# Optimization experiments

Hardware: AMD Instinct MI355X
Metric: run time of the kernel (lower is better)

Reference implementation:

```python
import jax, jax.numpy as jnp
import numpy as np

N = 50000          # nodes
E = 800000         # edges (avg degree 16)
NODE_IN, NODE_OUT = 64, 96
EDGE_IN, EDGE_OUT = 32, 32
CONV = [192, 192]  # hidden_conv_sizes
LIN = [192]        # hidden_linear_sizes
NUM_CLASSES = 2


def _linear_init(k, fan_in, fan_out):
    s = 1.0 / np.sqrt(fan_in)
    kw, kb = jax.random.split(k)
    W = jax.random.uniform(kw, (fan_in, fan_out), jnp.float32, -s, s)
    b = jax.random.uniform(kb, (fan_out,), jnp.float32, -s, s)
    return W, b


def setup_inputs() -> dict:
    key = jax.random.key(0)
    ks = jax.random.split(key, 10)
    node_feats = jax.random.normal(ks[0], (N, NODE_IN), jnp.float32)
    edge_feats = jax.random.normal(ks[1], (E, EDGE_IN), jnp.float32)
    src = jax.random.randint(ks[2], (E,), 0, N)
    dst = jax.random.randint(ks[3], (E,), 0, N)
    Wn, bn = _linear_init(ks[4], NODE_IN, NODE_OUT)
    We, be = _linear_init(ks[5], EDGE_IN, EDGE_OUT)
    Wc0, bc0 = _linear_init(ks[6], NODE_OUT + EDGE_OUT, CONV[0])
    Wc1, bc1 = _linear_init(ks[7], CONV[0], CONV[1])
    Wl0, bl0 = _linear_init(ks[8], CONV[1], LIN[0])
    Wo, bo = _linear_init(ks[9], LIN[0], NUM_CLASSES)
    return dict(node_feats=node_feats, edge_feats=edge_feats,
                Wn=Wn, bn=bn, We=We, be=be,
                Wc0=Wc0, bc0=bc0, Wc1=Wc1, bc1=bc1,
                Wl0=Wl0, bl0=bl0, Wo=Wo, bo=bo,
                src=src, dst=dst)


def reference(node_feats, edge_feats, Wn, bn, We, be, Wc0, bc0, Wc1, bc1,
              Wl0, bl0, Wo, bo, src, dst):
    ones = jnp.ones((E,), jnp.float32)
    deg_in = jnp.clip(jax.ops.segment_sum(ones, dst, num_segments=N), 1.0)
    deg_out = jnp.clip(jax.ops.segment_sum(ones, src, num_segments=N), 1.0)
    inv_in = jax.lax.rsqrt(deg_in)    # D_in^{-1/2}
    inv_out = jax.lax.rsqrt(deg_out)  # D_out^{-1/2}

    # EdgeLayer: per-edge linear, mean-aggregated onto destination nodes
    eh = edge_feats @ We + be                                   # [E, EDGE_OUT]
    edge_h = jax.nn.relu(
        jax.ops.segment_sum(eh, dst, num_segments=N) / deg_in[:, None])

    # NodeEmbeddingLayer: per-node linear
    node_h = jax.nn.relu(node_feats @ Wn + bn)                  # [N, NODE_OUT]

    h = jnp.concatenate([edge_h, node_h], axis=1)               # [N, EDGE_OUT+NODE_OUT]

    # dgl GraphConv (norm='both'): D_in^{-1/2} A D_out^{-1/2} h W + b
    # dropout is identity in eval mode
    for W, b in ((Wc0, bc0), (Wc1, bc1)):
        msg = (h * inv_out[:, None])[src]                       # [E, d] gather
        agg = jax.ops.segment_sum(msg, dst, num_segments=N) * inv_in[:, None]
        h = jax.nn.relu(agg @ W + b)

    h = jax.nn.relu(h @ Wl0 + bl0)
    return h @ Wo + bo                                          # [N, NUM_CLASSES]
```

## Files before the change

kernel.cpp:

```cpp
#include <hip/hip_runtime.h>

#define NN 50000
#define NE 800000
#define CAP 64

#define NPB 128
#define NBKT 391
#define NBKT_PAD 512
#define BCAP 3072
#define CHUNK 4096
#define GW4E 12500

typedef unsigned short u16;
typedef unsigned int u32;
typedef unsigned long long u64;
typedef __attribute__((ext_vector_type(8))) short bf8_t;
typedef __attribute__((ext_vector_type(4))) float f4_t;

__device__ __forceinline__ u16 f2b(float f) {
    unsigned u = __float_as_uint(f);
    unsigned r = u + 0x7FFF + ((u >> 16) & 1);
    return (u16)(r >> 16);
}

__device__ __forceinline__ void pack_one(const float* __restrict__ W, u16* __restrict__ Wp,
                                         int idx, int KS) {
    int l = idx & 63;
    int s = (idx >> 6) % KS;
    int t = (idx >> 6) / KS;
    int col = t * 16 + (l & 15);
    int krow = s * 32 + ((l >> 4) * 8);
    u16 tmp[8] __attribute__((aligned(16)));
#pragma unroll
    for (int j = 0; j < 8; ++j) tmp[j] = f2b(W[(size_t)(krow + j) * 192 + col]);
    *(uint4*)(Wp + (size_t)idx * 8) = *(const uint4*)tmp;
}

__global__ __launch_bounds__(256) void partition_pack_k(
    const int* __restrict__ src, const int* __restrict__ dst,
    int* __restrict__ deg_out, int* __restrict__ bktc,
    u64* __restrict__ part, int E,
    const float* __restrict__ Wc0, const float* __restrict__ Wc1,
    const float* __restrict__ Wl0,
    u16* __restrict__ Wp0, u16* __restrict__ Wp1, u16* __restrict__ Wp2) {
    const int PBLK = (E + CHUNK - 1) / CHUNK;
    if (blockIdx.x >= PBLK) {
        int idx = (blockIdx.x - PBLK) * 256 + threadIdx.x;
        if (idx < 3072) pack_one(Wc0, Wp0, idx, 4);
        else if (idx < 7680) pack_one(Wc1, Wp1, idx - 3072, 6);
        else if (idx < 12288) pack_one(Wl0, Wp2, idx - 7680, 6);
        return;
    }

    __shared__ unsigned cnt[NBKT_PAD];
    __shared__ unsigned base[NBKT_PAD];
    __shared__ unsigned cur[NBKT_PAD];
    __shared__ unsigned gbase[NBKT_PAD];
    __shared__ unsigned wtot[4];
    __shared__ u64 staged[CHUNK];

    const int tid = threadIdx.x;
    const int lane = tid & 63;
    const int wid = tid >> 6;
    const int e0 = blockIdx.x * CHUNK;
    const int n = min(CHUNK, E - e0);

    for (int i = tid; i < NBKT_PAD; i += 256) cnt[i] = 0;
    __syncthreads();

    for (int i = tid; i < n; i += 256) {
        int d = dst[e0 + i];
        atomicAdd(&cnt[d >> 7], 1u);
    }
    __syncthreads();

    {
        unsigned a = cnt[2 * tid];
        unsigned b = cnt[2 * tid + 1];
        unsigned ps = a + b;
        unsigned inc = ps;
#pragma unroll
        for (int d = 1; d < 64; d <<= 1) {
            unsigned v = __shfl_up(inc, d);
            if (lane >= d) inc += v;
        }
        if (lane == 63) wtot[wid] = inc;
        __syncthreads();
        unsigned wb = 0;
#pragma unroll
        for (int k = 0; k < 4; ++k) wb += (k < wid) ? wtot[k] : 0;
        unsigned eb = wb + inc - ps;
        base[2 * tid] = eb;
        base[2 * tid + 1] = eb + a;
        cur[2 * tid] = eb;
        cur[2 * tid + 1] = eb + a;
    }
    __syncthreads();

    for (int i = tid; i < n; i += 256) {
        int e = e0 + i;
        int d = dst[e];
        int s = src[e];
        atomicAdd(deg_out + s, 1);
        unsigned p = atomicAdd(&cur[d >> 7], 1u);
        staged[p] = ((u64)(unsigned)e << 32) | (((u32)d << 16) | (u32)s);
    }
    __syncthreads();

    for (int b = tid; b < NBKT; b += 256) {
        unsigned c = cur[b] - base[b];
        if (c) gbase[b] = (unsigned)atomicAdd(&bktc[b], (int)c);
    }
    __syncthreads();

    for (int i = tid; i < n; i += 256) {
        u64 v = staged[i];
        int b = (int)((v >> 16) & 0xffffu) >> 7;
        unsigned idx = gbase[b] + ((unsigned)i - base[b]);
        if (idx < BCAP) part[(size_t)b * BCAP + idx] = v;
    }
}

__global__ __launch_bounds__(256) void fill_k(
    const u64* __restrict__ part, const int* __restrict__ bktc,
    const int* __restrict__ deg_out,
    int* __restrict__ csr_src, int* __restrict__ csr_eid,
    int* __restrict__ din,
    float* __restrict__ inv_in, float* __restrict__ inv_out,
    float* __restrict__ inv_mean, float* __restrict__ bcoef, int n) {
    __shared__ unsigned cur[NPB];
    const int tid = threadIdx.x;
    const int b = blockIdx.x;
    const int node0 = b << 7;
    if (tid < NPB) cur[tid] = 0;
    __syncthreads();

    const int cnt = min(bktc[b], BCAP);
    const u64* p = part + (size_t)b * BCAP;
    for (int i = tid; i < cnt; i += 256) {
        u64 v = p[i];
        int s = (int)(v & 0xffffu);
        int d = (int)((v >> 16) & 0xffffu);
        int e = (int)(v >> 32);
        unsigned q = atomicAdd(&cur[d & (NPB - 1)], 1u);
        if (q < CAP) {
            csr_src[((size_t)d << 6) + q] = s;
            csr_eid[((size_t)d << 6) + q] = e;
        }
    }
    __syncthreads();
    if (tid < NPB) {
        int node = node0 + tid;
        if (node < n) {
            unsigned cq = min(cur[tid], (unsigned)CAP);
            din[node] = (int)cq;
            int end = (cq <= 32u) ? 32 : 64;
            for (int q = (int)cq; q < end; ++q)
                csr_eid[((size_t)node << 6) + q] = 0;
            float di = fmaxf((float)cq, 1.0f);
            float dq = fmaxf((float)deg_out[node], 1.0f);
            inv_in[node]   = 1.0f / sqrtf(di);
            inv_out[node]  = 1.0f / sqrtf(dq);
            inv_mean[node] = 1.0f / di;
            bcoef[node]    = (cq > 0u) ? 1.0f : 0.0f;
        }
    }
}

__global__ __launch_bounds__(256) void edge_node_k(
    const float* __restrict__ ef, const int* __restrict__ csr_eid,
    const int* __restrict__ deg,
    const float* __restrict__ inv_mean, const float* __restrict__ bcoef,
    const float* __restrict__ inv_out,
    const float* __restrict__ We, const float* __restrict__ be,
    const float* __restrict__ nf, const float* __restrict__ Wn,
    const float* __restrict__ bn,
    u16* __restrict__ h0, int n) {
    __shared__ float sv[4][32];
    __shared__ float s_in[32 * 64];
    const int tid = threadIdx.x;
    const int lane = tid & 63;
    const int w = tid >> 6;

    if (blockIdx.x < GW4E) {
        const int node = __builtin_amdgcn_readfirstlane(blockIdx.x * 4 + w);
        const int beg = node << 6;
        const int cnt = deg[node];
        const int g = lane >> 4;
        const int c = lane & 15;

        float ax = 0.0f, ay = 0.0f;
        {
            int eidv[8];
#pragma unroll
            for (int j = 0; j < 8; ++j) eidv[j] = csr_eid[beg + 4 * j + g];
            float2 v[8];
#pragma unroll
            for (int j = 0; j < 8; ++j)
                v[j] = *(const float2*)(ef + (size_t)eidv[j] * 32 + 2 * c);
#pragma unroll
            for (int j = 0; j < 8; ++j)
                if (4 * j + g < cnt) { ax += v[j].x; ay += v[j].y; }
        }
        if (cnt > 32) {
            int eidv[8];
#pragma unroll
            for (int j = 0; j < 8; ++j) eidv[j] = csr_eid[beg + 32 + 4 * j + g];
            float2 v[8];
#pragma unroll
            for (int j = 0; j < 8; ++j)
                v[j] = *(const float2*)(ef + (size_t)eidv[j] * 32 + 2 * c);
#pragma unroll
            for (int j = 0; j < 8; ++j)
                if (32 + 4 * j + g < cnt) { ax += v[j].x; ay += v[j].y; }
        }
        ax += __shfl_down(ax, 16); ay += __shfl_down(ay, 16);
        ax += __shfl_down(ax, 32); ay += __shfl_down(ay, 32);
        if (lane < 16) {
            float im = inv_mean[node];
            float2 o; o.x = ax * im; o.y = ay * im;
            *(float2*)&sv[w][2 * c] = o;
        }
        int col = lane & 31;
        float s = 0.0f;
#pragma unroll 8
        for (int k = 0; k < 32; ++k)
            s = fmaf(sv[w][k], We[k * 32 + col], s);
        if (lane < 32) {
            float v = fmaxf(s + be[col] * bcoef[node], 0.0f) * inv_out[node];
            h0[(size_t)node * 128 + col] = f2b(v);
        }
        return;
    }

    const int row0 = (blockIdx.x - GW4E) * 32;
    for (int i = tid; i < 512; i += 256) {
        int m = i >> 4;
        int kv = i & 15;
        int row = min(row0 + m, n - 1);
        float4 v = *(const float4*)(nf + (size_t)row * 64 + kv * 4);
        *(float4*)(s_in + m * 64 + kv * 4) = v;
    }
    __syncthreads();

    int f0 = lane, f1 = lane + 64;
    bool fok1 = (f1 < 96);
    int ff1 = fok1 ? f1 : 0;
    float bv0 = bn[f0], bv1 = bn[ff1];

    const float* s_my = s_in + w * 8 * 64;
    float acc0[8], acc1[8];
#pragma unroll
    for (int m = 0; m < 8; ++m) { acc0[m] = 0.0f; acc1[m] = 0.0f; }

    for (int k = 0; k < 64; k += 4) {
        float wv[4][2];
#pragma unroll
        for (int j = 0; j < 4; ++j) {
            wv[j][0] = Wn[(k + j) * 96 + f0];
            wv[j][1] = Wn[(k + j) * 96 + ff1];
        }
#pragma unroll
        for (int m = 0; m < 8; ++m) {
            float4 a = *(const float4*)(s_my + m * 64 + k);
            acc0[m] = fmaf(a.x, wv[0][0], acc0[m]);
            acc0[m] = fmaf(a.y, wv[1][0], acc0[m]);
            acc0[m] = fmaf(a.z, wv[2][0], acc0[m]);
            acc0[m] = fmaf(a.w, wv[3][0], acc0[m]);
            acc1[m] = fmaf(a.x, wv[0][1], acc1[m]);
            acc1[m] = fmaf(a.y, wv[1][1], acc1[m]);
            acc1[m] = fmaf(a.z, wv[2][1], acc1[m]);
            acc1[m] = fmaf(a.w, wv[3][1], acc1[m]);
        }
    }

#pragma unroll
    for (int m = 0; m < 8; ++m) {
        int row = row0 + w * 8 + m;
        if (row < n) {
            float pm = inv_out[row];
            float v0 = fmaxf(acc0[m] + bv0, 0.0f) * pm;
            h0[(size_t)row * 128 + 32 + f0] = f2b(v0);
            if (fok1) {
                float v1 = fmaxf(acc1[m] + bv1, 0.0f) * pm;
                h0[(size_t)row * 128 + 32 + f1] = f2b(v1);
            }
        }
    }
}

template <int D, int LPT>
__global__ __launch_bounds__(256) void gather_b2_k(
    const u16* __restrict__ h, const int* __restrict__ csr,
    const int* __restrict__ deg, const float* __restrict__ inv_in,
    u16* __restrict__ agg) {
    constexpr int ACT = D / LPT;
    constexpr int NW = LPT / 2;
    const int lane = threadIdx.x & 63;
    const int node = __builtin_amdgcn_readfirstlane(blockIdx.x * 4 + (threadIdx.x >> 6));
    const int beg = node << 6;
    const int cnt = deg[node];
    const int off = (lane < ACT ? lane : ACT - 1) * LPT;

    float acc[LPT];
#pragma unroll
    for (int j = 0; j < LPT; ++j) acc[j] = 0.0f;

    const int nb = cnt >> 4;
    int idx[16];
    if (nb > 0) {
#pragma unroll
        for (int j = 0; j < 16; ++j) idx[j] = csr[beg + j];
    }
    for (int b = 0; b < nb; ++b) {
        unsigned lv[16][NW];
#pragma unroll
        for (int j = 0; j < 16; ++j) {
            const unsigned* p = (const unsigned*)(h + (size_t)idx[j] * D + off);
            if constexpr (NW == 2) {
                uint2 t = *(const uint2*)p;
                lv[j][0] = t.x; lv[j][1] = t.y;
            } else {
                lv[j][0] = *p;
            }
        }
        int nidx[16];
        const int nbase = beg + (b + 1) * 16;
        if (b + 1 < nb) {
#pragma unroll
            for (int j = 0; j < 16; ++j) nidx[j] = csr[nbase + j];
        }
#pragma unroll
        for (int j = 0; j < 16; ++j)
#pragma unroll
            for (int q = 0; q < NW; ++q) {
                unsigned u = lv[j][q];
                acc[2 * q]     += __uint_as_float(u << 16);
                acc[2 * q + 1] += __uint_as_float(u & 0xffff0000u);
            }
        if (b + 1 < nb) {
#pragma unroll
            for (int j = 0; j < 16; ++j) idx[j] = nidx[j];
        }
    }

    int tb = beg + (nb << 4);
    int rem = cnt & 15;
    if (rem >= 8) {
        int ti[8];
#pragma unroll
        for (int j = 0; j < 8; ++j) ti[j] = csr[tb + j];
        unsigned lv[8][NW];
#pragma unroll
        for (int j = 0; j < 8; ++j) {
            const unsigned* p = (const unsigned*)(h + (size_t)ti[j] * D + off);
            if constexpr (NW == 2) {
                uint2 t = *(const uint2*)p;
                lv[j][0] = t.x; lv[j][1] = t.y;
            } else {
                lv[j][0] = *p;
            }
        }
#pragma unroll
        for (int j = 0; j < 8; ++j)
#pragma unroll
            for (int q = 0; q < NW; ++q) {
                unsigned u = lv[j][q];
                acc[2 * q]     += __uint_as_float(u << 16);
                acc[2 * q + 1] += __uint_as_float(u & 0xffff0000u);
            }
        tb += 8;
        rem -= 8;
    }
    for (int t = 0; t < rem; ++t) {
        const unsigned* p = (const unsigned*)(h + (size_t)csr[tb + t] * D + off);
#pragma unroll
        for (int q = 0; q < NW; ++q) {
            unsigned u = p[q];
            acc[2 * q]     += __uint_as_float(u << 16);
            acc[2 * q + 1] += __uint_as_float(u & 0xffff0000u);
        }
    }

    if (lane < ACT) {
        float sc = inv_in[node];
        unsigned o[NW];
#pragma unroll
        for (int q = 0; q < NW; ++q)
            o[q] = (unsigned)f2b(acc[2 * q] * sc) | ((unsigned)f2b(acc[2 * q + 1] * sc) << 16);
        unsigned* dp = (unsigned*)(agg + (size_t)node * D + off);
        if constexpr (NW == 2) {
            uint2 t; t.x = o[0]; t.y = o[1];
            *(uint2*)dp = t;
        } else {
            *dp = o[0];
        }
    }
}

template <int K>
__global__ __launch_bounds__(256) void mfma_gemm_k(
    const u16* __restrict__ A, const u16* __restrict__ Wp,
    const float* __restrict__ bias, const float* __restrict__ posts,
    u16* __restrict__ outB, int n) {
    constexpr int KS = K / 32;
    const int tid = threadIdx.x;
    const int lane = tid & 63;
    const int w = tid >> 6;
    const int row0 = blockIdx.x * 16;
    const int arow = row0 + (lane & 15);
    const int kbase = (lane >> 4) * 8;

    f4_t acc[3];
#pragma unroll
    for (int o = 0; o < 3; ++o) acc[o] = (f4_t){0.f, 0.f, 0.f, 0.f};

    const u16* ap = A + (size_t)arow * K + kbase;
#pragma unroll
    for (int s = 0; s < KS; ++s) {
        bf8_t af = *(const bf8_t*)(ap + s * 32);
#pragma unroll
        for (int o = 0; o < 3; ++o) {
            int t = w * 3 + o;
            bf8_t bf = *(const bf8_t*)(Wp + (size_t)((t * KS + s) * 64 + lane) * 8);
            acc[o] = __builtin_amdgcn_mfma_f32_16x16x32_bf16(af, bf, acc[o], 0, 0, 0);
        }
    }

    const int drow = row0 + (lane >> 4) * 4;
    const int dcol = lane & 15;
    float pm[4];
#pragma unroll
    for (int r = 0; r < 4; ++r) pm[r] = posts[drow + r];
#pragma unroll
    for (int o = 0; o < 3; ++o) {
        int col = (w * 3 + o) * 16 + dcol;
        float bv = bias[col];
#pragma unroll
        for (int r = 0; r < 4; ++r) {
            float v = fmaxf(acc[o][r] + bv, 0.0f) * pm[r];
            outB[(size_t)(drow + r) * 192 + col] = f2b(v);
        }
    }
}

__global__ __launch_bounds__(256) void mfma_fused_k(
    const u16* __restrict__ A,
    const u16* __restrict__ Wp1, const float* __restrict__ b1,
    const u16* __restrict__ Wp2, const float* __restrict__ b2,
    const float* __restrict__ Wo, const float* __restrict__ bo,
    float* __restrict__ out, int n) {
    constexpr int KS = 6;
    constexpr int S = 200;
    __shared__ float sbuf[16 * S];
    __shared__ float s_head[16][17][2];

    const int tid = threadIdx.x;
    const int lane = tid & 63;
    const int w = tid >> 6;
    const int row0 = blockIdx.x * 16;
    const int arow = row0 + (lane & 15);
    const int kbase = (lane >> 4) * 8;
    const int drow = (lane >> 4) * 4;
    const int dcol = lane & 15;

    f4_t acc[3];
#pragma unroll
    for (int o = 0; o < 3; ++o) acc[o] = (f4_t){0.f, 0.f, 0.f, 0.f};

    const u16* ap = A + (size_t)arow * 192 + kbase;
#pragma unroll
    for (int s = 0; s < KS; ++s) {
        bf8_t af = *(const bf8_t*)(ap + s * 32);
#pragma unroll
        for (int o = 0; o < 3; ++o) {
            int t = w * 3 + o;
            bf8_t bf = *(const bf8_t*)(Wp1 + (size_t)((t * KS + s) * 64 + lane) * 8);
            acc[o] = __builtin_amdgcn_mfma_f32_16x16x32_bf16(af, bf, acc[o], 0, 0, 0);
        }
    }

    u16* h2 = (u16*)sbuf;
#pragma unroll
    for (int o = 0; o < 3; ++o) {
        int col = (w * 3 + o) * 16 + dcol;
        float bv = b1[col];
#pragma unroll
        for (int r = 0; r < 4; ++r)
            h2[(drow + r) * S + col] = f2b(fmaxf(acc[o][r] + bv, 0.0f));
    }
    __syncthreads();

#pragma unroll
    for (int o = 0; o < 3; ++o) acc[o] = (f4_t){0.f, 0.f, 0.f, 0.f};
    const u16* hp = h2 + (lane & 15) * S + kbase;
#pragma unroll
    for (int s = 0; s < KS; ++s) {
        bf8_t af = *(const bf8_t*)(hp + s * 32);
#pragma unroll
        for (int o = 0; o < 3; ++o) {
            int t = w * 3 + o;
            bf8_t bf = *(const bf8_t*)(Wp2 + (size_t)((t * KS + s) * 64 + lane) * 8);
            acc[o] = __builtin_amdgcn_mfma_f32_16x16x32_bf16(af, bf, acc[o], 0, 0, 0);
        }
    }
    __syncthreads();

#pragma unroll
    for (int o = 0; o < 3; ++o) {
        int col = (w * 3 + o) * 16 + dcol;
        float bv = b2[col];
#pragma unroll
        for (int r = 0; r < 4; ++r)
            sbuf[(drow + r) * S + col] = fmaxf(acc[o][r] + bv, 0.0f);
    }
    __syncthreads();

    {
        int r = tid >> 4;
        int seg = tid & 15;
        const float* hr = sbuf + r * S + seg * 12;
        const float* wor = Wo + seg * 24;
        float p0 = 0.0f, p1 = 0.0f;
#pragma unroll
        for (int c = 0; c < 12; ++c) {
            float hv = hr[c];
            p0 = fmaf(hv, wor[c * 2 + 0], p0);
            p1 = fmaf(hv, wor[c * 2 + 1], p1);
        }
        s_head[r][seg][0] = p0;
        s_head[r][seg][1] = p1;
    }
    __syncthreads();
    if (tid < 32) {
        int r = tid >> 1, c = tid & 1;
        float sum = bo[c];
#pragma unroll
        for (int g = 0; g < 16; ++g) sum += s_head[r][g][c];
        int row = row0 + r;
        if (row < n) out[(size_t)row * 2 + c] = sum;
    }
}

extern "C" void kernel_launch(void* const* d_in, const int* in_sizes, int n_in,
                              void* d_out, int out_size, void* d_ws, size_t ws_size,
                              hipStream_t stream) {
    const float* node_feats = (const float*)d_in[0];
    const float* edge_feats = (const float*)d_in[1];
    const float* Wn  = (const float*)d_in[2];
    const float* bn  = (const float*)d_in[3];
    const float* We  = (const float*)d_in[4];
    const float* be  = (const float*)d_in[5];
    const float* Wc0 = (const float*)d_in[6];
    const float* bc0 = (const float*)d_in[7];
    const float* Wc1 = (const float*)d_in[8];
    const float* bc1 = (const float*)d_in[9];
    const float* Wl0 = (const float*)d_in[10];
    const float* bl0 = (const float*)d_in[11];
    const float* Wo  = (const float*)d_in[12];
    const float* bo  = (const float*)d_in[13];
    const int* src = (const int*)d_in[14];
    const int* dst = (const int*)d_in[15];
    float* out = (float*)d_out;

    const int N = NN, E = NE;

    int* dout      = (int*)d_ws;
    int* bktc      = dout + N;
    int* din       = bktc + NBKT_PAD;
    int* csr_src   = din + N;
    int* csr_eid   = csr_src + (size_t)CAP * N;
    float* inv_in   = (float*)(csr_eid + (size_t)CAP * N);
    float* inv_out  = inv_in + N;
    float* inv_mean = inv_out + N;
    float* bcoef    = inv_mean + N;
    u16* h0   = (u16*)(bcoef + N);
    u16* aggA = h0 + (size_t)128 * N;
    u16* h1   = aggA + (size_t)128 * N;
    u16* aggB = h1 + (size_t)192 * N;
    u16* Wp0  = aggB + (size_t)192 * N;
    u16* Wp1  = Wp0 + 128 * 192;
    u16* Wp2  = Wp1 + 192 * 192;
    u64* part = (u64*)h1;

    hipMemsetAsync(d_ws, 0, (size_t)(N + NBKT_PAD) * sizeof(int), stream);

    const int PBLK = (E + CHUNK - 1) / CHUNK;
    const int GB16 = N / 16;
    const int GB32 = (N + 31) / 32;

    partition_pack_k<<<dim3(PBLK + 48), dim3(256), 0, stream>>>(
        src, dst, dout, bktc, part, E, Wc0, Wc1, Wl0, Wp0, Wp1, Wp2);
    fill_k<<<dim3(NBKT), dim3(256), 0, stream>>>(part, bktc, dout, csr_src, csr_eid,
                                                 din, inv_in, inv_out, inv_mean, bcoef, N);

    edge_node_k<<<dim3(GW4E + GB32), dim3(256), 0, stream>>>(
        edge_feats, csr_eid, din, inv_mean, bcoef, inv_out, We, be,
        node_feats, Wn, bn, h0, N);

    gather_b2_k<128, 2><<<dim3(GW4E), dim3(256), 0, stream>>>(h0, csr_src, din, inv_in, aggA);
    mfma_gemm_k<128><<<dim3(GB16), dim3(256), 0, stream>>>(aggA, Wp0, bc0, inv_out, h1, N);

    gather_b2_k<192, 4><<<dim3(GW4E), dim3(256), 0, stream>>>(h1, csr_src, din, inv_in, aggB);
    mfma_fused_k<<<dim3(GB16), dim3(256), 0, stream>>>(aggB, Wp1, bc1, Wp2, bl0, Wo, bo,
                                                       out, N);
}
```

Before: 407.2 us.

## Fuse neighbor gather with MFMA GEMM per 16-node tile via shared memory

Merges each graph-conv gather kernel with its following MFMA GEMM into one 1024-thread block. Each of the 16 waves aggregates one node into an LDS tile, then 12 waves each compute one 16-column output slab. This removes the aggA/aggB intermediate round trips through global memory and two kernel launches. In exchange, the cross-iteration index prefetch is dropped, 4 waves sit idle during the GEMM phase, and the large blocks with barriers may lower occupancy and latency hiding for the irregular gathers.

New measurement: 424.6 us. 1.04x slower.

```diff
diff --git a/kernel.cpp b/kernel.cpp
--- a/kernel.cpp
+++ b/kernel.cpp
@@ -289,169 +289,100 @@
     }
 }
 
-template <int D, int LPT>
-__global__ __launch_bounds__(256) void gather_b2_k(
-    const u16* __restrict__ h, const int* __restrict__ csr,
+__global__ __launch_bounds__(1024) void conv0_k(
+    const u16* __restrict__ h0, const int* __restrict__ csr,
     const int* __restrict__ deg, const float* __restrict__ inv_in,
-    u16* __restrict__ agg) {
-    constexpr int ACT = D / LPT;
-    constexpr int NW = LPT / 2;
-    const int lane = threadIdx.x & 63;
-    const int node = __builtin_amdgcn_readfirstlane(blockIdx.x * 4 + (threadIdx.x >> 6));
-    const int beg = node << 6;
-    const int cnt = deg[node];
-    const int off = (lane < ACT ? lane : ACT - 1) * LPT;
-
-    float acc[LPT];
-#pragma unroll
-    for (int j = 0; j < LPT; ++j) acc[j] = 0.0f;
-
-    const int nb = cnt >> 4;
-    int idx[16];
-    if (nb > 0) {
-#pragma unroll
-        for (int j = 0; j < 16; ++j) idx[j] = csr[beg + j];
-    }
-    for (int b = 0; b < nb; ++b) {
-        unsigned lv[16][NW];
-#pragma unroll
-        for (int j = 0; j < 16; ++j) {
-            const unsigned* p = (const unsigned*)(h + (size_t)idx[j] * D + off);
-            if constexpr (NW == 2) {
-                uint2 t = *(const uint2*)p;
-                lv[j][0] = t.x; lv[j][1] = t.y;
-            } else {
-                lv[j][0] = *p;
-            }
-        }
-        int nidx[16];
-        const int nbase = beg + (b + 1) * 16;
-        if (b + 1 < nb) {
-#pragma unroll
-            for (int j = 0; j < 16; ++j) nidx[j] = csr[nbase + j];
-        }
-#pragma unroll
-        for (int j = 0; j < 16; ++j)
-#pragma unroll
-            for (int q = 0; q < NW; ++q) {
-                unsigned u = lv[j][q];
-                acc[2 * q]     += __uint_as_float(u << 16);
-                acc[2 * q + 1] += __uint_as_float(u & 0xffff0000u);
-            }
-        if (b + 1 < nb) {
-#pragma unroll
-            for (int j = 0; j < 16; ++j) idx[j] = nidx[j];
-        }
-    }
-
-    int tb = beg + (nb << 4);
-    int rem = cnt & 15;
-    if (rem >= 8) {
-        int ti[8];
-#pragma unroll
-        for (int j = 0; j < 8; ++j) ti[j] = csr[tb + j];
-        unsigned lv[8][NW];
-#pragma unroll
-        for (int j = 0; j < 8; ++j) {
-            const unsigned* p = (const unsigned*)(h + (size_t)ti[j] * D + off);
-            if constexpr (NW == 2) {
-                uint2 t = *(const uint2*)p;
-                lv[j][0] = t.x; lv[j][1] = t.y;
-            } else {
-                lv[j][0] = *p;
-            }
-        }
-#pragma unroll
-        for (int j = 0; j < 8; ++j)
-#pragma unroll
-            for (int q = 0; q < NW; ++q) {
-                unsigned u = lv[j][q];
-                acc[2 * q]     += __uint_as_float(u << 16);
-                acc[2 * q + 1] += __uint_as_float(u & 0xffff0000u);
-            }
-        tb += 8;
-        rem -= 8;
-    }
-    for (int t = 0; t < rem; ++t) {
-        const unsigned* p = (const unsigned*)(h + (size_t)csr[tb + t] * D + off);
-#pragma unroll
-        for (int q = 0; q < NW; ++q) {
-            unsigned u = p[q];
-            acc[2 * q]     += __uint_as_float(u << 16);
-            acc[2 * q + 1] += __uint_as_float(u & 0xffff0000u);
-        }
-    }
-
-    if (lane < ACT) {
-        float sc = inv_in[node];
-        unsigned o[NW];
-#pragma unroll
-        for (int q = 0; q < NW; ++q)
-            o[q] = (unsigned)f2b(acc[2 * q] * sc) | ((unsigned)f2b(acc[2 * q + 1] * sc) << 16);
-        unsigned* dp = (unsigned*)(agg + (size_t)node * D + off);
-        if constexpr (NW == 2) {
-            uint2 t; t.x = o[0]; t.y = o[1];
-            *(uint2*)dp = t;
-        } else {
-            *dp = o[0];
-        }
-    }
-}
-
-template <int K>
-__global__ __launch_bounds__(256) void mfma_gemm_k(
-    const u16* __restrict__ A, const u16* __restrict__ Wp,
-    const float* __restrict__ bias, const float* __restrict__ posts,
-    u16* __restrict__ outB, int n) {
-    constexpr int KS = K / 32;
+    const u16* __restrict__ Wp, const float* __restrict__ bias,
+    const float* __restrict__ posts, u16* __restrict__ h1) {
+    constexpr int KS = 4, ST = 136;
+    __shared__ u16 tile[16 * ST];
     const int tid = threadIdx.x;
     const int lane = tid & 63;
     const int w = tid >> 6;
     const int row0 = blockIdx.x * 16;
-    const int arow = row0 + (lane & 15);
-    const int kbase = (lane >> 4) * 8;
-
-    f4_t acc[3];
-#pragma unroll
-    for (int o = 0; o < 3; ++o) acc[o] = (f4_t){0.f, 0.f, 0.f, 0.f};
-
-    const u16* ap = A + (size_t)arow * K + kbase;
-#pragma unroll
-    for (int s = 0; s < KS; ++s) {
-        bf8_t af = *(const bf8_t*)(ap + s * 32);
-#pragma unroll
-        for (int o = 0; o < 3; ++o) {
-            int t = w * 3 + o;
-            bf8_t bf = *(const bf8_t*)(Wp + (size_t)((t * KS + s) * 64 + lane) * 8);
-            acc[o] = __builtin_amdgcn_mfma_f32_16x16x32_bf16(af, bf, acc[o], 0, 0, 0);
-        }
-    }
-
-    const int drow = row0 + (lane >> 4) * 4;
-    const int dcol = lane & 15;
-    float pm[4];
-#pragma unroll
-    for (int r = 0; r < 4; ++r) pm[r] = posts[drow + r];
-#pragma unroll
-    for (int o = 0; o < 3; ++o) {
-        int col = (w * 3 + o) * 16 + dcol;
+    const int node = __builtin_amdgcn_readfirstlane(row0 + w);
+    const int beg = node << 6;
+    const int cnt = deg[node];
+    const int off = lane * 2;
+
+    float a0 = 0.0f, a1 = 0.0f;
+    {
+        const int nb = cnt >> 4;
+        for (int b = 0; b < nb; ++b) {
+            int idx[16];
+#pragma unroll
+            for (int j = 0; j < 16; ++j) idx[j] = csr[beg + b * 16 + j];
+            unsigned lv[16];
+#pragma unroll
+            for (int j = 0; j < 16; ++j)
+                lv[j] = *(const unsigned*)(h0 + (size_t)idx[j] * 128 + off);
+#pragma unroll
+            for (int j = 0; j < 16; ++j) {
+                a0 += __uint_as_float(lv[j] << 16);
+                a1 += __uint_as_float(lv[j] & 0xffff0000u);
+            }
+        }
+        int tb = beg + (nb << 4);
+        int rem = cnt & 15;
+        if (rem >= 8) {
+            int ti[8];
+#pragma unroll
+            for (int j = 0; j < 8; ++j) ti[j] = csr[tb + j];
+            unsigned lv[8];
+#pragma unroll
+            for (int j = 0; j < 8; ++j)
+                lv[j] = *(const unsigned*)(h0 + (size_t)ti[j] * 128 + off);
+#pragma unroll
+            for (int j = 0; j < 8; ++j) {
+                a0 += __uint_as_float(lv[j] << 16);
+                a1 += __uint_as_float(lv[j] & 0xffff0000u);
+            }
+            tb += 8; rem -= 8;
+        }
+        for (int t = 0; t < rem; ++t) {
+            unsigned u = *(const unsigned*)(h0 + (size_t)csr[tb + t] * 128 + off);
+            a0 += __uint_as_float(u << 16);
+            a1 += __uint_as_float(u & 0xffff0000u);
+        }
+    }
+    {
+        float sc = inv_in[node];
+        unsigned o = (unsigned)f2b(a0 * sc) | ((unsigned)f2b(a1 * sc) << 16);
+        *(unsigned*)&tile[w * ST + off] = o;
+    }
+    __syncthreads();
+
+    if (w < 12) {
+        const int kbase = (lane >> 4) * 8;
+        f4_t acc = (f4_t){0.f, 0.f, 0.f, 0.f};
+        const u16* ap = tile + (lane & 15) * ST + kbase;
+#pragma unroll
+        for (int s = 0; s < KS; ++s) {
+            bf8_t af = *(const bf8_t*)(ap + s * 32);
+            bf8_t bf = *(const bf8_t*)(Wp + (size_t)((w * KS + s) * 64 + lane) * 8);
+            acc = __builtin_amdgcn_mfma_f32_16x16x32_bf16(af, bf, acc, 0, 0, 0);
+        }
+        const int drow = row0 + (lane >> 4) * 4;
+        const int dcol = lane & 15;
+        const int col = w * 16 + dcol;
         float bv = bias[col];
 #pragma unroll
         for (int r = 0; r < 4; ++r) {
-            float v = fmaxf(acc[o][r] + bv, 0.0f) * pm[r];
-            outB[(size_t)(drow + r) * 192 + col] = f2b(v);
-        }
-    }
-}
-
-__global__ __launch_bounds__(256) void mfma_fused_k(
-    const u16* __restrict__ A,
+            float v = fmaxf(acc[r] + bv, 0.0f) * posts[drow + r];
+            h1[(size_t)(drow + r) * 192 + col] = f2b(v);
+        }
+    }
+}
+
+__global__ __launch_bounds__(1024) void conv1_k(
+    const u16* __restrict__ h1, const int* __restrict__ csr,
+    const int* __restrict__ deg, const float* __restrict__ inv_in,
     const u16* __restrict__ Wp1, const float* __restrict__ b1,
     const u16* __restrict__ Wp2, const float* __restrict__ b2,
     const float* __restrict__ Wo, const float* __restrict__ bo,
     float* __restrict__ out, int n) {
-    constexpr int KS = 6;
-    constexpr int S = 200;
+    constexpr int KS = 6, S = 200;
+    __shared__ u16 tileA[16 * S];
     __shared__ float sbuf[16 * S];
     __shared__ float s_head[16][17][2];
 
@@ -459,64 +390,119 @@
     const int lane = tid & 63;
     const int w = tid >> 6;
     const int row0 = blockIdx.x * 16;
-    const int arow = row0 + (lane & 15);
+    const int node = __builtin_amdgcn_readfirstlane(row0 + w);
+    const int beg = node << 6;
+    const int cnt = deg[node];
+    const int goff = (lane < 48 ? lane : 47) * 4;
     const int kbase = (lane >> 4) * 8;
     const int drow = (lane >> 4) * 4;
     const int dcol = lane & 15;
 
-    f4_t acc[3];
-#pragma unroll
-    for (int o = 0; o < 3; ++o) acc[o] = (f4_t){0.f, 0.f, 0.f, 0.f};
-
-    const u16* ap = A + (size_t)arow * 192 + kbase;
-#pragma unroll
-    for (int s = 0; s < KS; ++s) {
-        bf8_t af = *(const bf8_t*)(ap + s * 32);
-#pragma unroll
-        for (int o = 0; o < 3; ++o) {
-            int t = w * 3 + o;
-            bf8_t bf = *(const bf8_t*)(Wp1 + (size_t)((t * KS + s) * 64 + lane) * 8);
-            acc[o] = __builtin_amdgcn_mfma_f32_16x16x32_bf16(af, bf, acc[o], 0, 0, 0);
-        }
-    }
+    {
+        float acc4[4];
+#pragma unroll
+        for (int j = 0; j < 4; ++j) acc4[j] = 0.0f;
+        const int nb = cnt >> 4;
+        for (int b = 0; b < nb; ++b) {
+            int idx[16];
+#pragma unroll
+            for (int j = 0; j < 16; ++j) idx[j] = csr[beg + b * 16 + j];
+            unsigned lv[16][2];
+#pragma unroll
+            for (int j = 0; j < 16; ++j) {
+                uint2 t = *(const uint2*)(h1 + (size_t)idx[j] * 192 + goff);
+                lv[j][0] = t.x; lv[j][1] = t.y;
+            }
+#pragma unroll
+            for (int j = 0; j < 16; ++j)
+#pragma unroll
+                for (int q = 0; q < 2; ++q) {
+                    unsigned u = lv[j][q];
+                    acc4[2 * q]     += __uint_as_float(u << 16);
+                    acc4[2 * q + 1] += __uint_as_float(u & 0xffff0000u);
+                }
+        }
+        int tb = beg + (nb << 4);
+        int rem = cnt & 15;
+        if (rem >= 8) {
+            int ti[8];
+#pragma unroll
+            for (int j = 0; j < 8; ++j) ti[j] = csr[tb + j];
+            unsigned lv[8][2];
+#pragma unroll
+            for (int j = 0; j < 8; ++j) {
+                uint2 t = *(const uint2*)(h1 + (size_t)ti[j] * 192 + goff);
+                lv[j][0] = t.x; lv[j][1] = t.y;
+            }
+#pragma unroll
+            for (int j = 0; j < 8; ++j)
+#pragma unroll
+                for (int q = 0; q < 2; ++q) {
+                    unsigned u = lv[j][q];
+                    acc4[2 * q]     += __uint_as_float(u << 16);
+                    acc4[2 * q + 1] += __uint_as_float(u & 0xffff0000u);
+                }
+            tb += 8; rem -= 8;
+        }
+        for (int t = 0; t < rem; ++t) {
+            const unsigned* p = (const unsigned*)(h1 + (size_t)csr[tb + t] * 192 + goff);
+#pragma unroll
+            for (int q = 0; q < 2; ++q) {
+                unsigned u = p[q];
+                acc4[2 * q]     += __uint_as_float(u << 16);
+                acc4[2 * q + 1] += __uint_as_float(u & 0xffff0000u);
+            }
+        }
+        if (lane < 48) {
+            float sc = inv_in[node];
+            uint2 o;
+            o.x = (unsigned)f2b(acc4[0] * sc) | ((unsigned)f2b(acc4[1] * sc) << 16);
+            o.y = (unsigned)f2b(acc4[2] * sc) | ((unsigned)f2b(acc4[3] * sc) << 16);
+            *(uint2*)&tileA[w * S + goff] = o;
+        }
+    }
+    __syncthreads();
 
     u16* h2 = (u16*)sbuf;
-#pragma unroll
-    for (int o = 0; o < 3; ++o) {
-        int col = (w * 3 + o) * 16 + dcol;
+    if (w < 12) {
+        f4_t acc = (f4_t){0.f, 0.f, 0.f, 0.f};
+        const u16* ap = tileA + (lane & 15) * S + kbase;
+#pragma unroll
+        for (int s = 0; s < KS; ++s) {
+            bf8_t af = *(const bf8_t*)(ap + s * 32);
+            bf8_t bf = *(const bf8_t*)(Wp1 + (size_t)((w * KS + s) * 64 + lane) * 8);
+            acc = __builtin_amdgcn_mfma_f32_16x16x32_bf16(af, bf, acc, 0, 0, 0);
+        }
+        int col = w * 16 + dcol;
         float bv = b1[col];
 #pragma unroll
         for (int r = 0; r < 4; ++r)
-            h2[(drow + r) * S + col] = f2b(fmaxf(acc[o][r] + bv, 0.0f));
-    }
-    __syncthreads();
-
-#pragma unroll
-    for (int o = 0; o < 3; ++o) acc[o] = (f4_t){0.f, 0.f, 0.f, 0.f};
-    const u16* hp = h2 + (lane & 15) * S + kbase;
-#pragma unroll
-    for (int s = 0; s < KS; ++s) {
-        bf8_t af = *(const bf8_t*)(hp + s * 32);
-#pragma unroll
-        for (int o = 0; o < 3; ++o) {
-            int t = w * 3 + o;
-            bf8_t bf = *(const bf8_t*)(Wp2 + (size_t)((t * KS + s) * 64 + lane) * 8);
-            acc[o] = __builtin_amdgcn_mfma_f32_16x16x32_bf16(af, bf, acc[o], 0, 0, 0);
-        }
-    }
-    __syncthreads();
-
-#pragma unroll
-    for (int o = 0; o < 3; ++o) {
-        int col = (w * 3 + o) * 16 + dcol;
+            h2[(drow + r) * S + col] = f2b(fmaxf(acc[r] + bv, 0.0f));
+    }
+    __syncthreads();
+
+    f4_t acc2 = (f4_t){0.f, 0.f, 0.f, 0.f};
+    if (w < 12) {
+        const u16* hp = h2 + (lane & 15) * S + kbase;
+#pragma unroll
+        for (int s = 0; s < KS; ++s) {
+            bf8_t af = *(const bf8_t*)(hp + s * 32);
+            bf8_t bf = *(const bf8_t*)(Wp2 + (size_t)((w * KS + s) * 64 + lane) * 8);
+            acc2 = __builtin_amdgcn_mfma_f32_16x16x32_bf16(af, bf, acc2, 0, 0, 0);
+        }
+    }
+    __syncthreads();
+
+    if (w < 12) {
+        int col = w * 16 + dcol;
         float bv = b2[col];
 #pragma unroll
         for (int r = 0; r < 4; ++r)
-            sbuf[(drow + r) * S + col] = fmaxf(acc[o][r] + bv, 0.0f);
-    }
-    __syncthreads();
-
-    {
+            sbuf[(drow + r) * S + col] = fmaxf(acc2[r] + bv, 0.0f);
+    }
+    __syncthreads();
+
+    if (tid < 256) {
         int r = tid >> 4;
         int seg = tid & 15;
         const float* hr = sbuf + r * S + seg * 12;
@@ -575,10 +561,8 @@
     float* inv_mean = inv_out + N;
     float* bcoef    = inv_mean + N;
     u16* h0   = (u16*)(bcoef + N);
-    u16* aggA = h0 + (size_t)128 * N;
-    u16* h1   = aggA + (size_t)128 * N;
-    u16* aggB = h1 + (size_t)192 * N;
-    u16* Wp0  = aggB + (size_t)192 * N;
+    u16* h1   = h0 + (size_t)128 * N;
+    u16* Wp0  = h1 + (size_t)192 * N;
     u16* Wp1  = Wp0 + 128 * 192;
     u16* Wp2  = Wp1 + 192 * 192;
     u64* part = (u64*)h1;
@@ -598,10 +582,8 @@
         edge_feats, csr_eid, din, inv_mean, bcoef, inv_out, We, be,
         node_feats, Wn, bn, h0, N);
 
-    gather_b2_k<128, 2><<<dim3(GW4E), dim3(256), 0, stream>>>(h0, csr_src, din, inv_in, aggA);
-    mfma_gemm_k<128><<<dim3(GB16), dim3(256), 0, stream>>>(aggA, Wp0, bc0, inv_out, h1, N);
-
-    gather_b2_k<192, 4><<<dim3(GW4E), dim3(256), 0, stream>>>(h1, csr_src, din, inv_in, aggB);
-    mfma_fused_k<<<dim3(GB16), dim3(256), 0, stream>>>(aggB, Wp1, bc1, Wp2, bl0, Wo, bo,
-                                                       out, N);
-}
+    conv0_k<<<dim3(GB16), dim3(1024), 0, stream>>>(h0, csr_src, din, inv_in,
+                                                   Wp0, bc0, inv_out, h1);
+    conv1_k<<<dim3(GB16), dim3(1024), 0, stream>>>(h1, csr_src, din, inv_in,
+                                                   Wp1, bc1, Wp2, bl0, Wo, bo, out, N);
+}
```
